# Kernel tuning notes

Hardware: AMD Instinct MI355X
Metric: run time of the kernel (lower is better)

The kernel has to match this reference:

```python
import jax, jax.numpy as jnp
import numpy as np

B, N, F_IN, F_OUT = 16, 4096, 64, 64


def setup_inputs() -> dict:
    key = jax.random.key(0)
    k1, k2, k3, k4 = jax.random.split(key, 4)
    stdv = 1.0 / np.sqrt(F_OUT)
    graph = jax.random.normal(k1, (B, N, F_IN), dtype=jnp.float32)
    adj = jax.random.uniform(k2, (N, N), dtype=jnp.float32)
    weight = jax.random.uniform(k3, (F_IN, F_OUT), minval=-stdv, maxval=stdv, dtype=jnp.float32)
    bias = jax.random.uniform(k4, (F_OUT,), minval=-stdv, maxval=stdv, dtype=jnp.float32)
    return {"graph": graph, "adj": adj, "weight": weight, "bias": bias}


def _normalize_adj(adj):
    # Symmetric normalization D^{-1/2} A D^{-1/2}.
    # diag_embed @ adj @ diag_embed == row/col elementwise scaling (same math, O(N^2)).
    rowsum = jnp.sum(adj, axis=-1)
    rowsum = rowsum + (rowsum == 0).astype(adj.dtype)  # avoid div-by-zero for isolated nodes
    d_inv_sqrt = rowsum ** -0.5
    return d_inv_sqrt[:, None] * adj * d_inv_sqrt[None, :]


def reference(graph, adj, weight, bias):
    adj_norm = _normalize_adj(adj)                      # [N, N]
    support = jnp.einsum('bni,io->bno', graph, weight)  # [B, N, F_out]
    output = jnp.einsum('nm,bmo->bno', adj_norm, support)
    output = jax.nn.relu(output + bias)
    return (output, adj)
```

## Files before the change

kernel.cpp:

```cpp
#include <hip/hip_runtime.h>
#include <hip/hip_bf16.h>
#include <stdint.h>


typedef __bf16 bf16;
typedef __bf16 bf16x4 __attribute__((ext_vector_type(4)));
typedef __bf16 bf16x8 __attribute__((ext_vector_type(8)));
typedef float f32x4 __attribute__((ext_vector_type(4)));

#define NN 4096
#define BATCH 16
#define FD 64
#define CDIM 1024

__global__ __launch_bounds__(256) void k_prep(const float* __restrict__ adj,
                                              bf16* __restrict__ adjb,
                                              float* __restrict__ dsq,
                                              float4* __restrict__ out1,
                                              int do_copy) {
    int row = blockIdx.x;
    const float4* p = (const float4*)(adj + (size_t)row * NN);
    uint4* q = (uint4*)(adjb + (size_t)row * NN);
    float4* o = out1 + (size_t)row * (NN / 4);
    float s = 0.f;
    for (int j = threadIdx.x; j < 512; j += 256) {
        float4 a = p[2 * j], b = p[2 * j + 1];
        if (do_copy) { o[2 * j] = a; o[2 * j + 1] = b; }
        bf16x8 h;
        h[0] = (bf16)a.x; h[1] = (bf16)a.y; h[2] = (bf16)a.z; h[3] = (bf16)a.w;
        h[4] = (bf16)b.x; h[5] = (bf16)b.y; h[6] = (bf16)b.z; h[7] = (bf16)b.w;
        q[j] = __builtin_bit_cast(uint4, h);
        s += a.x + a.y + a.z + a.w + b.x + b.y + b.z + b.w;
    }
    #pragma unroll
    for (int off = 32; off > 0; off >>= 1) s += __shfl_down(s, off, 64);
    __shared__ float red[4];
    int lane = threadIdx.x & 63, wv = threadIdx.x >> 6;
    if (lane == 0) red[wv] = s;
    __syncthreads();
    if (threadIdx.x == 0) {
        float t = red[0] + red[1] + red[2] + red[3];
        if (t == 0.f) t = 1.f;
        dsq[row] = 1.0f / sqrtf(t);
    }
}

__global__ __launch_bounds__(256) void k_support(const float* __restrict__ graph,
                                                 const float* __restrict__ weight,
                                                 const float* __restrict__ dsq,
                                                 bf16* __restrict__ spT) {
    __shared__ float wT[64 * 64];
    int tid = threadIdx.x;
    for (int idx = tid; idx < 4096; idx += 256) {
        int i = idx >> 6, o = idx & 63;
        wT[o * 64 + i] = weight[idx];
    }
    __syncthreads();
    int b = blockIdx.y;
    int m = blockIdx.x * 256 + tid;
    const float4* g4 = (const float4*)(graph + ((size_t)b * NN + m) * FD);
    float ds = dsq[m];
    float gr[64];
    #pragma unroll
    for (int j = 0; j < 16; j++) {
        float4 v = g4[j];
        gr[4 * j] = v.x * ds; gr[4 * j + 1] = v.y * ds;
        gr[4 * j + 2] = v.z * ds; gr[4 * j + 3] = v.w * ds;
    }
    bf16* outp = spT + m;
    for (int o = 0; o < 64; o++) {
        const float4* w4 = (const float4*)&wT[o * 64];
        float acc = 0.f;
        #pragma unroll
        for (int j = 0; j < 16; j++) {
            float4 wv = w4[j];
            acc += gr[4 * j] * wv.x + gr[4 * j + 1] * wv.y
                 + gr[4 * j + 2] * wv.z + gr[4 * j + 3] * wv.w;
        }
        outp[(size_t)(b * 64 + o) * NN] = (bf16)acc;
    }
}

__global__ __launch_bounds__(256, 4) void k_gemm(const bf16* __restrict__ adjb,
                                                 const bf16* __restrict__ spT,
                                                 const float* __restrict__ dsq,
                                                 bf16* __restrict__ part,
                                                 int kchunk) {
    __shared__ bf16x8 lds_a[1024];
    __shared__ bf16x8 lds_b[1024];
    const int tid = threadIdx.x;
    const int lane = tid & 63;
    const int w = tid >> 6;
    const int n0 = blockIdx.x * 128;
    const int c0 = blockIdx.y * 128;
    const size_t kbase = (size_t)blockIdx.z * kchunk;
    const int niter = kchunk >> 6;
    bf16* __restrict__ pp = part + (size_t)blockIdx.z * NN * CDIM;

    const bf16* gA[4]; const bf16* gB[4];
    bf16x8* lA[4]; bf16x8* lB[4];
    #pragma unroll
    for (int j = 0; j < 4; j++) {
        int g = (w * 4 + j) * 64 + lane;
        int row = g >> 3;
        int sub = (g & 7) ^ (row & 7);
        gA[j] = adjb + (size_t)(n0 + row) * NN + kbase + sub * 8;
        gB[j] = spT  + (size_t)(c0 + row) * NN + kbase + sub * 8;
        lA[j] = &lds_a[(w * 4 + j) * 64];
        lB[j] = &lds_b[(w * 4 + j) * 64];
    }

    const int r = lane & 15, qo = lane >> 4;
    const int rm = (w >> 1) * 64, rc = (w & 1) * 64;
    const int rowA = rm + r, rowB = rc + r;
    const bf16x8* fA0 = lds_a + rowA * 8 + ((qo)     ^ (rowA & 7));
    const bf16x8* fA1 = lds_a + rowA * 8 + ((4 + qo) ^ (rowA & 7));
    const bf16x8* fB0 = lds_b + rowB * 8 + ((qo)     ^ (rowB & 7));
    const bf16x8* fB1 = lds_b + rowB * 8 + ((4 + qo) ^ (rowB & 7));

    f32x4 ac[4][4];
    #pragma unroll
    for (int i = 0; i < 4; i++)
        #pragma unroll
        for (int j = 0; j < 4; j++)
            ac[i][j] = (f32x4){0.f, 0.f, 0.f, 0.f};

    for (int it = 0; it < niter; it++) {
        const int kt = it * 64;
        __syncthreads();
        #pragma unroll
        for (int j = 0; j < 4; j++) {
            __builtin_amdgcn_global_load_lds(
                (const __attribute__((address_space(1))) void*)(gA[j] + kt),
                (__attribute__((address_space(3))) void*)lA[j], 16, 0, 0);
            __builtin_amdgcn_global_load_lds(
                (const __attribute__((address_space(1))) void*)(gB[j] + kt),
                (__attribute__((address_space(3))) void*)lB[j], 16, 0, 0);
        }
        __syncthreads();
        {
            bf16x8 af[4], bfr[4];
            #pragma unroll
            for (int mi = 0; mi < 4; mi++) af[mi] = fA0[mi * 128];
            #pragma unroll
            for (int ni = 0; ni < 4; ni++) bfr[ni] = fB0[ni * 128];
            #pragma unroll
            for (int mi = 0; mi < 4; mi++)
                #pragma unroll
                for (int ni = 0; ni < 4; ni++)
                    ac[mi][ni] = __builtin_amdgcn_mfma_f32_16x16x32_bf16(
                        af[mi], bfr[ni], ac[mi][ni], 0, 0, 0);
        }
        {
            bf16x8 af[4], bfr[4];
            #pragma unroll
            for (int mi = 0; mi < 4; mi++) af[mi] = fA1[mi * 128];
            #pragma unroll
            for (int ni = 0; ni < 4; ni++) bfr[ni] = fB1[ni * 128];
            #pragma unroll
            for (int mi = 0; mi < 4; mi++)
                #pragma unroll
                for (int ni = 0; ni < 4; ni++)
                    ac[mi][ni] = __builtin_amdgcn_mfma_f32_16x16x32_bf16(
                        af[mi], bfr[ni], ac[mi][ni], 0, 0, 0);
        }
    }

    #pragma unroll
    for (int mi = 0; mi < 4; mi++) {
        float dn[4];
        #pragma unroll
        for (int rr = 0; rr < 4; rr++) dn[rr] = dsq[n0 + rm + mi * 16 + qo * 4 + rr];
        #pragma unroll
        for (int ni = 0; ni < 4; ni++) {
            int c = c0 + rc + ni * 16 + r;
            #pragma unroll
            for (int rr = 0; rr < 4; rr++) {
                int n = n0 + rm + mi * 16 + qo * 4 + rr;
                pp[(size_t)n * CDIM + c] = (bf16)(dn[rr] * ac[mi][ni][rr]);
            }
        }
    }
}

__global__ __launch_bounds__(256) void k_epi(const bf16* __restrict__ part,
                                             int nsplit,
                                             const float* __restrict__ bias,
                                             float4* __restrict__ out0) {
    int idx = blockIdx.x * 256 + threadIdx.x;
    int flat = idx * 4;
    int o4 = flat & 63;
    int n = (flat >> 6) & (NN - 1);
    int b = flat >> 18;
    size_t off = (size_t)n * CDIM + b * 64 + o4;
    const size_t zstride = (size_t)NN * CDIM;
    float ax = 0.f, ay = 0.f, az = 0.f, aw = 0.f;
    for (int z = 0; z < nsplit; z++) {
        bf16x4 t = *(const bf16x4*)(part + off + z * zstride);
        ax += (float)t[0]; ay += (float)t[1]; az += (float)t[2]; aw += (float)t[3];
    }
    float4 bv = *(const float4*)(bias + o4);
    float4 r;
    r.x = fmaxf(ax + bv.x, 0.f);
    r.y = fmaxf(ay + bv.y, 0.f);
    r.z = fmaxf(az + bv.z, 0.f);
    r.w = fmaxf(aw + bv.w, 0.f);
    out0[idx] = r;
}

__global__ __launch_bounds__(256) void k_copy(const float4* __restrict__ src,
                                              float4* __restrict__ dst) {
    size_t i = (size_t)blockIdx.x * 256 + threadIdx.x;
    dst[i] = src[i];
}

extern "C" void kernel_launch(void* const* d_in, const int* in_sizes, int n_in,
                              void* d_out, int out_size, void* d_ws, size_t ws_size,
                              hipStream_t stream) {
    const float *graph = nullptr, *adj = nullptr, *weight = nullptr, *bias = nullptr;
    for (int i = 0; i < n_in; i++) {
        const float* p = (const float*)d_in[i];
        switch (in_sizes[i]) {
            case BATCH * NN * FD: graph  = p; break;
            case NN * NN:         adj    = p; break;
            case FD * FD:         weight = p; break;
            case FD:              bias   = p; break;
        }
    }

    float* out0 = (float*)d_out;
    float* out1 = out0 + (size_t)BATCH * NN * FD;

    const size_t SZ_ADJB = (size_t)NN * NN * 2;
    const size_t SZ_SPT  = (size_t)CDIM * NN * 2;
    const size_t SZ_DSQ  = (size_t)NN * 4;
    const size_t SZ_PART = (size_t)NN * CDIM * 2;

    bf16 *adjb, *spT, *part; float *dsq;
    int nsplit, do_copy_in_prep;
    if (ws_size >= SZ_ADJB + SZ_SPT + SZ_DSQ + 4 * SZ_PART) {
        nsplit = 4; do_copy_in_prep = 1;
        char* s = (char*)d_ws;
        adjb = (bf16*)s;
        spT  = (bf16*)(s + SZ_ADJB);
        dsq  = (float*)(s + SZ_ADJB + SZ_SPT);
        part = (bf16*)(s + SZ_ADJB + SZ_SPT + SZ_DSQ);
    } else if (ws_size >= SZ_ADJB + SZ_SPT + SZ_DSQ + 2 * SZ_PART) {
        nsplit = 2; do_copy_in_prep = 1;
        char* s = (char*)d_ws;
        adjb = (bf16*)s;
        spT  = (bf16*)(s + SZ_ADJB);
        dsq  = (float*)(s + SZ_ADJB + SZ_SPT);
        part = (bf16*)(s + SZ_ADJB + SZ_SPT + SZ_DSQ);
    } else {
        nsplit = 4; do_copy_in_prep = 0;
        part = (bf16*)out1;
        adjb = (bf16*)((char*)out1 + 4 * SZ_PART);
        spT  = (bf16*)out0;
        dsq  = (float*)((char*)out0 + SZ_SPT);
    }
    const int kchunk = NN / nsplit;

    hipLaunchKernelGGL(k_prep, dim3(NN), dim3(256), 0, stream,
                       adj, adjb, dsq, (float4*)out1, do_copy_in_prep);
    hipLaunchKernelGGL(k_support, dim3(16, 16), dim3(256), 0, stream,
                       graph, weight, dsq, spT);
    hipLaunchKernelGGL(k_gemm, dim3(32, 8, nsplit), dim3(256), 0, stream,
                       adjb, spT, dsq, part, kchunk);
    hipLaunchKernelGGL(k_epi, dim3(4096), dim3(256), 0, stream,
                       part, nsplit, bias, (float4*)out0);
    if (!do_copy_in_prep) {
        hipLaunchKernelGGL(k_copy, dim3(16384), dim3(256), 0, stream,
                           (const float4*)adj, (float4*)out1);
    }
}
```

Measured before the change: 223.1 us.

## Enlarge GEMM tile to 256x256 with double-buffered LDS and ping-pong scheduling

The adjacency GEMM now uses 512-thread blocks computing 256x256 output tiles, with each wave covering 128x64. LDS is double-buffered so the next K-slice is prefetched with global_load_lds while MFMAs run on the current buffer. Barriers and s_setprio interleave the fragment loads and MFMA phases. This is meant to raise arithmetic intensity and hide global-memory latency, at the cost of more registers (128 accumulators), more LDS per block (128 KB), and fewer blocks in the grid (512 with nsplit=8, 256 with nsplit=4).

```diff
diff --git a/kernel.cpp b/kernel.cpp
--- a/kernel.cpp
+++ b/kernel.cpp
@@ -81,102 +81,151 @@
     }
 }
 
-__global__ __launch_bounds__(256, 4) void k_gemm(const bf16* __restrict__ adjb,
+__global__ __launch_bounds__(512, 2) void k_gemm(const bf16* __restrict__ adjb,
                                                  const bf16* __restrict__ spT,
                                                  const float* __restrict__ dsq,
                                                  bf16* __restrict__ part,
                                                  int kchunk) {
-    __shared__ bf16x8 lds_a[1024];
-    __shared__ bf16x8 lds_b[1024];
+    __shared__ bf16x8 lds_a[2][2048];
+    __shared__ bf16x8 lds_b[2][2048];
     const int tid = threadIdx.x;
     const int lane = tid & 63;
     const int w = tid >> 6;
-    const int n0 = blockIdx.x * 128;
-    const int c0 = blockIdx.y * 128;
+    const int wr = w >> 2, wc = w & 3;
+    const int r = lane & 15, qo = lane >> 4;
+    const int n0 = blockIdx.x * 256;
+    const int c0 = blockIdx.y * 256;
     const size_t kbase = (size_t)blockIdx.z * kchunk;
-    const int niter = kchunk >> 6;
+    const int nt = kchunk >> 6;
     bf16* __restrict__ pp = part + (size_t)blockIdx.z * NN * CDIM;
 
     const bf16* gA[4]; const bf16* gB[4];
-    bf16x8* lA[4]; bf16x8* lB[4];
     #pragma unroll
     for (int j = 0; j < 4; j++) {
-        int g = (w * 4 + j) * 64 + lane;
+        int g = j * 512 + tid;
         int row = g >> 3;
         int sub = (g & 7) ^ (row & 7);
         gA[j] = adjb + (size_t)(n0 + row) * NN + kbase + sub * 8;
         gB[j] = spT  + (size_t)(c0 + row) * NN + kbase + sub * 8;
-        lA[j] = &lds_a[(w * 4 + j) * 64];
-        lB[j] = &lds_b[(w * 4 + j) * 64];
-    }
-
-    const int r = lane & 15, qo = lane >> 4;
-    const int rm = (w >> 1) * 64, rc = (w & 1) * 64;
-    const int rowA = rm + r, rowB = rc + r;
-    const bf16x8* fA0 = lds_a + rowA * 8 + ((qo)     ^ (rowA & 7));
-    const bf16x8* fA1 = lds_a + rowA * 8 + ((4 + qo) ^ (rowA & 7));
-    const bf16x8* fB0 = lds_b + rowB * 8 + ((qo)     ^ (rowB & 7));
-    const bf16x8* fB1 = lds_b + rowB * 8 + ((4 + qo) ^ (rowB & 7));
-
-    f32x4 ac[4][4];
-    #pragma unroll
-    for (int i = 0; i < 4; i++)
+    }
+
+    const int rowA0 = wr * 128 + r;
+    const int rowB0 = wc * 64 + r;
+    const int cc  = qo ^ (r & 7);
+    const int aoff  = rowA0 * 8 + cc;
+    const int aoff4 = rowA0 * 8 + (cc ^ 4);
+    const int boff  = rowB0 * 8 + cc;
+    const int boff4 = rowB0 * 8 + (cc ^ 4);
+
+    f32x4 ac[8][4];
+    #pragma unroll
+    for (int i = 0; i < 8; i++)
         #pragma unroll
         for (int j = 0; j < 4; j++)
             ac[i][j] = (f32x4){0.f, 0.f, 0.f, 0.f};
 
-    for (int it = 0; it < niter; it++) {
-        const int kt = it * 64;
-        __syncthreads();
-        #pragma unroll
-        for (int j = 0; j < 4; j++) {
-            __builtin_amdgcn_global_load_lds(
-                (const __attribute__((address_space(1))) void*)(gA[j] + kt),
-                (__attribute__((address_space(3))) void*)lA[j], 16, 0, 0);
-            __builtin_amdgcn_global_load_lds(
-                (const __attribute__((address_space(1))) void*)(gB[j] + kt),
-                (__attribute__((address_space(3))) void*)lB[j], 16, 0, 0);
-        }
-        __syncthreads();
-        {
-            bf16x8 af[4], bfr[4];
+    bf16x8 a_[4][2];
+    bf16x8 b_[2][2];
+
+#define GLL(gp, lp) __builtin_amdgcn_global_load_lds( \
+        (const __attribute__((address_space(1))) void*)(gp), \
+        (__attribute__((address_space(3))) void*)(lp), 16, 0, 0)
+
+#define LDA(mh) { _Pragma("unroll") \
+    for (int mi = 0; mi < 4; mi++) { \
+        a_[mi][0] = fa[aoff  + (mh) * 512 + mi * 128]; \
+        a_[mi][1] = fa[aoff4 + (mh) * 512 + mi * 128]; \
+    } }
+
+#define LDB(np) { _Pragma("unroll") \
+    for (int u = 0; u < 2; u++) { \
+        b_[u][0] = fb[boff  + ((np) * 2 + u) * 128]; \
+        b_[u][1] = fb[boff4 + ((np) * 2 + u) * 128]; \
+    } }
+
+#define MM(mh, np) { _Pragma("unroll") \
+    for (int mi = 0; mi < 4; mi++) { \
+        _Pragma("unroll") \
+        for (int u = 0; u < 2; u++) { \
+            ac[(mh)*4+mi][(np)*2+u] = __builtin_amdgcn_mfma_f32_16x16x32_bf16( \
+                a_[mi][0], b_[u][0], ac[(mh)*4+mi][(np)*2+u], 0, 0, 0); \
+            ac[(mh)*4+mi][(np)*2+u] = __builtin_amdgcn_mfma_f32_16x16x32_bf16( \
+                a_[mi][1], b_[u][1], ac[(mh)*4+mi][(np)*2+u], 0, 0, 0); \
+        } } }
+
+    #pragma unroll
+    for (int j = 0; j < 4; j++) {
+        GLL(gA[j], &lds_a[0][j * 512 + (w << 6)]);
+        GLL(gB[j], &lds_b[0][j * 512 + (w << 6)]);
+    }
+    asm volatile("s_waitcnt vmcnt(0)" ::: "memory");
+    __builtin_amdgcn_s_barrier();
+    asm volatile("" ::: "memory");
+
+    for (int t = 0; t < nt; t++) {
+        const bf16x8* fa = lds_a[t & 1];
+        const bf16x8* fb = lds_b[t & 1];
+        bf16x8* sa = lds_a[(t + 1) & 1];
+        bf16x8* sb = lds_b[(t + 1) & 1];
+        const int toff = (t + 1) * 64;
+        const bool st = (t + 1 < nt);
+
+        LDA(0); LDB(0);
+        if (st) {
             #pragma unroll
-            for (int mi = 0; mi < 4; mi++) af[mi] = fA0[mi * 128];
+            for (int j = 0; j < 4; j++) GLL(gA[j] + toff, &sa[j * 512 + (w << 6)]);
+        }
+        __builtin_amdgcn_s_barrier();
+        __builtin_amdgcn_s_setprio(1);
+        MM(0, 0);
+        __builtin_amdgcn_s_setprio(0);
+        __builtin_amdgcn_s_barrier();
+
+        LDB(1);
+        if (st) {
             #pragma unroll
-            for (int ni = 0; ni < 4; ni++) bfr[ni] = fB0[ni * 128];
-            #pragma unroll
-            for (int mi = 0; mi < 4; mi++)
-                #pragma unroll
-                for (int ni = 0; ni < 4; ni++)
-                    ac[mi][ni] = __builtin_amdgcn_mfma_f32_16x16x32_bf16(
-                        af[mi], bfr[ni], ac[mi][ni], 0, 0, 0);
-        }
-        {
-            bf16x8 af[4], bfr[4];
-            #pragma unroll
-            for (int mi = 0; mi < 4; mi++) af[mi] = fA1[mi * 128];
-            #pragma unroll
-            for (int ni = 0; ni < 4; ni++) bfr[ni] = fB1[ni * 128];
-            #pragma unroll
-            for (int mi = 0; mi < 4; mi++)
-                #pragma unroll
-                for (int ni = 0; ni < 4; ni++)
-                    ac[mi][ni] = __builtin_amdgcn_mfma_f32_16x16x32_bf16(
-                        af[mi], bfr[ni], ac[mi][ni], 0, 0, 0);
-        }
-    }
-
-    #pragma unroll
-    for (int mi = 0; mi < 4; mi++) {
+            for (int j = 0; j < 4; j++) GLL(gB[j] + toff, &sb[j * 512 + (w << 6)]);
+        }
+        __builtin_amdgcn_s_barrier();
+        __builtin_amdgcn_s_setprio(1);
+        MM(0, 1);
+        __builtin_amdgcn_s_setprio(0);
+        __builtin_amdgcn_s_barrier();
+
+        LDA(1);
+        __builtin_amdgcn_s_barrier();
+        __builtin_amdgcn_s_setprio(1);
+        MM(1, 1);
+        __builtin_amdgcn_s_setprio(0);
+        __builtin_amdgcn_s_barrier();
+
+        LDB(0);
+        __builtin_amdgcn_s_barrier();
+        __builtin_amdgcn_s_setprio(1);
+        MM(1, 0);
+        __builtin_amdgcn_s_setprio(0);
+        if (st) asm volatile("s_waitcnt vmcnt(0)" ::: "memory");
+        __builtin_amdgcn_s_barrier();
+        asm volatile("" ::: "memory");
+    }
+
+#undef GLL
+#undef LDA
+#undef LDB
+#undef MM
+
+    #pragma unroll
+    for (int mi = 0; mi < 8; mi++) {
         float dn[4];
         #pragma unroll
-        for (int rr = 0; rr < 4; rr++) dn[rr] = dsq[n0 + rm + mi * 16 + qo * 4 + rr];
+        for (int rr = 0; rr < 4; rr++)
+            dn[rr] = dsq[n0 + wr * 128 + mi * 16 + qo * 4 + rr];
         #pragma unroll
         for (int ni = 0; ni < 4; ni++) {
-            int c = c0 + rc + ni * 16 + r;
+            int c = c0 + wc * 64 + ni * 16 + r;
             #pragma unroll
             for (int rr = 0; rr < 4; rr++) {
-                int n = n0 + rm + mi * 16 + qo * 4 + rr;
+                int n = n0 + wr * 128 + mi * 16 + qo * 4 + rr;
                 pp[(size_t)n * CDIM + c] = (bf16)(dn[rr] * ac[mi][ni][rr]);
             }
         }
@@ -265,7 +314,7 @@
                        adj, adjb, dsq, (float4*)out1, do_copy_in_prep);
     hipLaunchKernelGGL(k_support, dim3(16, 16), dim3(256), 0, stream,
                        graph, weight, dsq, spT);
-    hipLaunchKernelGGL(k_gemm, dim3(32, 8, nsplit), dim3(256), 0, stream,
+    hipLaunchKernelGGL(k_gemm, dim3(16, 4, nsplit), dim3(512), 0, stream,
                        adjb, spT, dsq, part, kchunk);
     hipLaunchKernelGGL(k_epi, dim3(4096), dim3(256), 0, stream,
                        part, nsplit, bias, (float4*)out0);
```

After: 230.3 us. +3.2%, slower.

## Rewrite bf16 GEMM as 256x256-tile, 8-wave, double-buffered pipelined kernel

Applied to the files above, without the earlier changes.

The aggregation GEMM moves from 128x128 tiles with 4 waves and a single LDS buffer to 256x256 tiles with 8 waves and double-buffered LDS split into K-halves. Global-to-LDS async loads for the next stage are interleaved with the MFMA phases using explicit vmcnt waits, barriers and s_setprio, so memory latency overlaps compute and each loaded tile is reused more. The cost is a much smaller grid (16x4xnsplit blocks), which may leave CUs underused, plus larger LDS and register pressure from 128 accumulators per thread.

```diff
diff --git a/kernel.cpp b/kernel.cpp
--- a/kernel.cpp
+++ b/kernel.cpp
@@ -81,102 +81,135 @@
     }
 }
 
-__global__ __launch_bounds__(256, 4) void k_gemm(const bf16* __restrict__ adjb,
+__global__ __launch_bounds__(512, 2) void k_gemm(const bf16* __restrict__ adjb,
                                                  const bf16* __restrict__ spT,
                                                  const float* __restrict__ dsq,
                                                  bf16* __restrict__ part,
                                                  int kchunk) {
-    __shared__ bf16x8 lds_a[1024];
-    __shared__ bf16x8 lds_b[1024];
+    __shared__ bf16x8 lds_a[2][2][1024];
+    __shared__ bf16x8 lds_b[2][2][1024];
     const int tid = threadIdx.x;
     const int lane = tid & 63;
     const int w = tid >> 6;
-    const int n0 = blockIdx.x * 128;
-    const int c0 = blockIdx.y * 128;
+    const int wr = w >> 2, wc = w & 3;
+    const int r = lane & 15, qo = lane >> 4;
+    const int n0 = blockIdx.x * 256;
+    const int c0 = blockIdx.y * 256;
     const size_t kbase = (size_t)blockIdx.z * kchunk;
-    const int niter = kchunk >> 6;
+    const int nt = kchunk >> 6;
     bf16* __restrict__ pp = part + (size_t)blockIdx.z * NN * CDIM;
 
-    const bf16* gA[4]; const bf16* gB[4];
-    bf16x8* lA[4]; bf16x8* lB[4];
-    #pragma unroll
-    for (int j = 0; j < 4; j++) {
-        int g = (w * 4 + j) * 64 + lane;
-        int row = g >> 3;
-        int sub = (g & 7) ^ (row & 7);
+    const bf16* gA[2]; const bf16* gB[2]; int ldso[2];
+    #pragma unroll
+    for (int j = 0; j < 2; j++) {
+        int g = (j * 8 + w) * 64 + lane;
+        int row = g >> 2;
+        int sub = (g & 3) ^ ((row >> 1) & 3);
         gA[j] = adjb + (size_t)(n0 + row) * NN + kbase + sub * 8;
         gB[j] = spT  + (size_t)(c0 + row) * NN + kbase + sub * 8;
-        lA[j] = &lds_a[(w * 4 + j) * 64];
-        lB[j] = &lds_b[(w * 4 + j) * 64];
-    }
-
-    const int r = lane & 15, qo = lane >> 4;
-    const int rm = (w >> 1) * 64, rc = (w & 1) * 64;
-    const int rowA = rm + r, rowB = rc + r;
-    const bf16x8* fA0 = lds_a + rowA * 8 + ((qo)     ^ (rowA & 7));
-    const bf16x8* fA1 = lds_a + rowA * 8 + ((4 + qo) ^ (rowA & 7));
-    const bf16x8* fB0 = lds_b + rowB * 8 + ((qo)     ^ (rowB & 7));
-    const bf16x8* fB1 = lds_b + rowB * 8 + ((4 + qo) ^ (rowB & 7));
-
-    f32x4 ac[4][4];
-    #pragma unroll
-    for (int i = 0; i < 4; i++)
+        ldso[j] = (j * 8 + w) * 64;
+    }
+
+    const int co = qo ^ ((r >> 1) & 3);
+    const int aidx = (wr * 128 + r) * 4 + co;
+    const int bidx = (wc * 64 + r) * 4 + co;
+
+    f32x4 ac[8][4];
+    #pragma unroll
+    for (int i = 0; i < 8; i++)
         #pragma unroll
         for (int j = 0; j < 4; j++)
             ac[i][j] = (f32x4){0.f, 0.f, 0.f, 0.f};
 
-    for (int it = 0; it < niter; it++) {
-        const int kt = it * 64;
-        __syncthreads();
-        #pragma unroll
-        for (int j = 0; j < 4; j++) {
-            __builtin_amdgcn_global_load_lds(
-                (const __attribute__((address_space(1))) void*)(gA[j] + kt),
-                (__attribute__((address_space(3))) void*)lA[j], 16, 0, 0);
-            __builtin_amdgcn_global_load_lds(
-                (const __attribute__((address_space(1))) void*)(gB[j] + kt),
-                (__attribute__((address_space(3))) void*)lB[j], 16, 0, 0);
+    bf16x8 a_[4], b_[4];
+
+#define GLL(gp, lp) __builtin_amdgcn_global_load_lds( \
+        (const __attribute__((address_space(1))) void*)(gp), \
+        (__attribute__((address_space(3))) void*)(lp), 16, 0, 0)
+#define STGA(bf_, kh, kt) { _Pragma("unroll") \
+    for (int j = 0; j < 2; j++) GLL(gA[j] + (kt) + (kh) * 32, &lds_a[bf_][kh][ldso[j]]); }
+#define STGB(bf_, kh, kt) { _Pragma("unroll") \
+    for (int j = 0; j < 2; j++) GLL(gB[j] + (kt) + (kh) * 32, &lds_b[bf_][kh][ldso[j]]); }
+#define DSA(c_, kk, mh) { _Pragma("unroll") \
+    for (int mi = 0; mi < 4; mi++) a_[mi] = lds_a[c_][kk][aidx + (mh) * 256 + mi * 64]; }
+#define DSB(c_, kk) { _Pragma("unroll") \
+    for (int ni = 0; ni < 4; ni++) b_[ni] = lds_b[c_][kk][bidx + ni * 64]; }
+#define MM(mh) { _Pragma("unroll") \
+    for (int mi = 0; mi < 4; mi++) { _Pragma("unroll") \
+        for (int ni = 0; ni < 4; ni++) \
+            ac[(mh) * 4 + mi][ni] = __builtin_amdgcn_mfma_f32_16x16x32_bf16( \
+                a_[mi], b_[ni], ac[(mh) * 4 + mi][ni], 0, 0, 0); } }
+#define BAR() __builtin_amdgcn_s_barrier()
+#define PRIO1() __builtin_amdgcn_s_setprio(1)
+#define PRIO0() __builtin_amdgcn_s_setprio(0)
+
+    STGA(0, 0, 0); STGB(0, 0, 0);
+    STGA(0, 1, 0); STGB(0, 1, 0);
+    STGA(1, 0, 64); STGB(1, 0, 64);
+    asm volatile("s_waitcnt vmcnt(8)" ::: "memory");
+    BAR();
+
+    for (int t = 0; t < nt - 1; t++) {
+        const int c = t & 1;
+        const int kt1 = (t + 1) * 64, kt2 = (t + 2) * 64;
+        DSA(c, 0, 0); DSB(c, 0);
+        STGA(c ^ 1, 1, kt1);
+        BAR(); PRIO1(); MM(0); PRIO0(); BAR();
+        DSA(c, 0, 1);
+        STGB(c ^ 1, 1, kt1);
+        BAR(); PRIO1(); MM(1); PRIO0();
+        asm volatile("s_waitcnt vmcnt(8)" ::: "memory");
+        BAR();
+        DSA(c, 1, 0); DSB(c, 1);
+        if (t < nt - 2) STGA(c, 0, kt2);
+        BAR(); PRIO1(); MM(0); PRIO0(); BAR();
+        DSA(c, 1, 1);
+        if (t < nt - 2) STGB(c, 0, kt2);
+        BAR(); PRIO1(); MM(1); PRIO0();
+        if (t < nt - 2) {
+            asm volatile("s_waitcnt vmcnt(8)" ::: "memory");
+        } else {
+            asm volatile("s_waitcnt vmcnt(4)" ::: "memory");
         }
-        __syncthreads();
-        {
-            bf16x8 af[4], bfr[4];
-            #pragma unroll
-            for (int mi = 0; mi < 4; mi++) af[mi] = fA0[mi * 128];
-            #pragma unroll
-            for (int ni = 0; ni < 4; ni++) bfr[ni] = fB0[ni * 128];
-            #pragma unroll
-            for (int mi = 0; mi < 4; mi++)
-                #pragma unroll
-                for (int ni = 0; ni < 4; ni++)
-                    ac[mi][ni] = __builtin_amdgcn_mfma_f32_16x16x32_bf16(
-                        af[mi], bfr[ni], ac[mi][ni], 0, 0, 0);
-        }
-        {
-            bf16x8 af[4], bfr[4];
-            #pragma unroll
-            for (int mi = 0; mi < 4; mi++) af[mi] = fA1[mi * 128];
-            #pragma unroll
-            for (int ni = 0; ni < 4; ni++) bfr[ni] = fB1[ni * 128];
-            #pragma unroll
-            for (int mi = 0; mi < 4; mi++)
-                #pragma unroll
-                for (int ni = 0; ni < 4; ni++)
-                    ac[mi][ni] = __builtin_amdgcn_mfma_f32_16x16x32_bf16(
-                        af[mi], bfr[ni], ac[mi][ni], 0, 0, 0);
-        }
-    }
-
-    #pragma unroll
-    for (int mi = 0; mi < 4; mi++) {
+        BAR();
+    }
+
+    {
+        const int c = (nt - 1) & 1;
+        DSA(c, 0, 0); DSB(c, 0);
+        BAR(); PRIO1(); MM(0); PRIO0(); BAR();
+        DSA(c, 0, 1);
+        BAR(); PRIO1(); MM(1); PRIO0();
+        asm volatile("s_waitcnt vmcnt(0)" ::: "memory");
+        BAR();
+        DSA(c, 1, 0); DSB(c, 1);
+        BAR(); PRIO1(); MM(0); PRIO0(); BAR();
+        DSA(c, 1, 1);
+        BAR(); PRIO1(); MM(1); PRIO0();
+    }
+
+#undef GLL
+#undef STGA
+#undef STGB
+#undef DSA
+#undef DSB
+#undef MM
+#undef BAR
+#undef PRIO1
+#undef PRIO0
+
+    #pragma unroll
+    for (int mi = 0; mi < 8; mi++) {
         float dn[4];
         #pragma unroll
-        for (int rr = 0; rr < 4; rr++) dn[rr] = dsq[n0 + rm + mi * 16 + qo * 4 + rr];
+        for (int rr = 0; rr < 4; rr++)
+            dn[rr] = dsq[n0 + wr * 128 + mi * 16 + qo * 4 + rr];
         #pragma unroll
         for (int ni = 0; ni < 4; ni++) {
-            int c = c0 + rc + ni * 16 + r;
+            int c = c0 + wc * 64 + ni * 16 + r;
             #pragma unroll
             for (int rr = 0; rr < 4; rr++) {
-                int n = n0 + rm + mi * 16 + qo * 4 + rr;
+                int n = n0 + wr * 128 + mi * 16 + qo * 4 + rr;
                 pp[(size_t)n * CDIM + c] = (bf16)(dn[rr] * ac[mi][ni][rr]);
             }
         }
@@ -265,7 +298,7 @@
                        adj, adjb, dsq, (float4*)out1, do_copy_in_prep);
     hipLaunchKernelGGL(k_support, dim3(16, 16), dim3(256), 0, stream,
                        graph, weight, dsq, spT);
-    hipLaunchKernelGGL(k_gemm, dim3(32, 8, nsplit), dim3(256), 0, stream,
+    hipLaunchKernelGGL(k_gemm, dim3(16, 4, nsplit), dim3(512), 0, stream,
                        adjb, spT, dsq, part, kchunk);
     hipLaunchKernelGGL(k_epi, dim3(4096), dim3(256), 0, stream,
                        part, nsplit, bias, (float4*)out0);
```

Result: slower. 231.4 us (+3.7%).
